# Performance work log

Hardware: AMD Instinct MI355X
Metric: run time of the kernel (lower is better)

Reference implementation:

```python
import jax, jax.numpy as jnp
import numpy as np

NUM_RULES = 256
IN_F = 2048
OUT_F = 2048
RANK = 8
BLOCK = 64
NUM_BLOCKS = min(IN_F, OUT_F) // BLOCK  # 32
SHARED_RANK = int(round(np.sqrt(min(IN_F, OUT_F))))  # 45
N = 16384


def setup_inputs() -> dict:
    key = jax.random.key(0)
    ks = jax.random.split(key, 7)
    x = jax.random.normal(ks[0], (N, IN_F), dtype=jnp.float32)
    rule_ids = jax.random.randint(ks[1], (N,), 0, NUM_RULES, dtype=jnp.int32)
    shared_in = jax.random.normal(ks[2], (IN_F, SHARED_RANK), dtype=jnp.float32) * (1.0 / np.sqrt(IN_F))
    shared_out = jax.random.normal(ks[3], (SHARED_RANK, OUT_F), dtype=jnp.float32) * (1.0 / np.sqrt(SHARED_RANK))
    rule_in = jax.random.normal(ks[4], (NUM_RULES, BLOCK, RANK), dtype=jnp.float32) * (1.0 / np.sqrt(BLOCK))
    rule_out = jax.random.normal(ks[5], (NUM_RULES, RANK, BLOCK), dtype=jnp.float32) * (1.0 / np.sqrt(RANK))
    rule_block_logits = jax.random.normal(ks[6], (NUM_RULES, NUM_BLOCKS), dtype=jnp.float32) * (1.0 / np.sqrt(NUM_BLOCKS))
    return {"x": x, "rule_ids": rule_ids, "shared_in": shared_in, "shared_out": shared_out,
            "rule_in": rule_in, "rule_out": rule_out, "rule_block_logits": rule_block_logits}


def reference(x, rule_ids, shared_in, shared_out, rule_in, rule_out, rule_block_logits):
    # Shared low-rank path: [N, in] @ [in, r] @ [r, out]
    base_out = (x @ shared_in) @ shared_out  # [N, OUT_F]

    total = NUM_BLOCKS * BLOCK
    x_blocks = x[:, :total].reshape(-1, NUM_BLOCKS, BLOCK)  # [N, B, bs]

    # Per-token gather of rule adapter params. This is mathematically
    # identical to the torch sort/pad/bmm/scatter path (zero padding
    # contributes zero), expressed as a dense gather + batched einsum.
    r_in = rule_in[rule_ids]    # [N, bs, RANK]
    r_out = rule_out[rule_ids]  # [N, RANK, bs]
    hidden = jnp.einsum('nbs,nsr->nbr', x_blocks, r_in)     # [N, B, RANK]
    adapter = jnp.einsum('nbr,nrs->nbs', hidden, r_out)     # [N, B, bs]

    # Block selector softmax with temperature 1/sqrt(num_blocks)
    inv_temp = jnp.sqrt(jnp.float32(NUM_BLOCKS))
    sel = jax.nn.softmax(rule_block_logits[rule_ids] * inv_temp, axis=-1)  # [N, B]
    weighted = (adapter * sel[:, :, None]).reshape(-1, total)  # [N, total]

    adapter_full = jnp.zeros_like(base_out).at[:, :total].set(weighted.astype(base_out.dtype))
    return base_out + adapter_full
```

## Files before the change

kernel.cpp:

```cpp
#include <hip/hip_runtime.h>
#include <hip/hip_bf16.h>
#include <math.h>

#define NTOK  16384
#define INF   2048
#define OUTF  2048
#define SR    45
#define RANK  8
#define BLK   64
#define NBLK  32
#define NRULE 256
#define NHIST 32
#define MAXSLOT (NTOK + NRULE * 15)
#define NTILE32 (MAXSLOT / 32)

typedef __attribute__((ext_vector_type(8))) short bf16x8;
typedef __attribute__((ext_vector_type(4))) float f32x4;
typedef __attribute__((ext_vector_type(4))) short s16x4;

typedef const __attribute__((address_space(1))) unsigned int GU32;
typedef __attribute__((address_space(3))) unsigned int LU32;

#define MFMA __builtin_amdgcn_mfma_f32_16x16x32_bf16
#define SBAR() __builtin_amdgcn_sched_barrier(0)

__device__ inline short f2bs(float f) {
    __hip_bfloat16 h = __float2bfloat16(f);
    return *reinterpret_cast<short*>(&h);
}
__device__ inline bf16x8 cvt8(const float4& a, const float4& b) {
    bf16x8 r;
    r[0] = f2bs(a.x); r[1] = f2bs(a.y); r[2] = f2bs(a.z); r[3] = f2bs(a.w);
    r[4] = f2bs(b.x); r[5] = f2bs(b.y); r[6] = f2bs(b.z); r[7] = f2bs(b.w);
    return r;
}

__global__ void kprep_a(const int* __restrict__ rule_ids,
                        const float* __restrict__ shared_in,
                        const float* __restrict__ shared_out,
                        const float* __restrict__ rule_in,
                        const float* __restrict__ rule_out,
                        unsigned short* __restrict__ ssb,
                        unsigned short* __restrict__ sob,
                        unsigned short* __restrict__ rinf,
                        unsigned short* __restrict__ rof,
                        int* __restrict__ ghist_part,
                        int* __restrict__ perm_p,
                        int* __restrict__ srid_p)
{
    if (blockIdx.x < 128) {
        const int tid = blockIdx.x * 256 + threadIdx.x;
        const int stride = 128 * 256;
        for (int idx = tid; idx < 64 * 3 * 512; idx += stride) {
            int ch = idx / 1536, rem = idx - ch * 1536;
            int nf = rem / 512;
            int l = (rem >> 3) & 63, j = idx & 7;
            int k = ch * 32 + ((l >> 4) << 3) + j;
            int col = nf * 16 + (l & 15);
            ssb[idx] = (col < SR) ? (unsigned short)f2bs(shared_in[(size_t)k * SR + col]) : 0;
        }
        for (int idx = tid; idx < 128 * 2 * 512; idx += stride) {
            int CF = idx >> 10;
            int kc = (idx >> 9) & 1;
            int l = (idx >> 3) & 63, j = idx & 7;
            int k = kc * 32 + ((l >> 4) << 3) + j;
            int col = CF * 16 + (l & 15);
            sob[idx] = (k < SR) ? (unsigned short)f2bs(shared_out[(size_t)k * OUTF + col]) : 0;
        }
        for (int idx = tid; idx < NRULE * 2 * 512; idx += stride) {
            int rid = idx >> 10;
            int half = (idx >> 9) & 1;
            int l = (idx >> 3) & 63, j = idx & 7;
            int r = l & 15;
            int s = half * 32 + ((l >> 4) << 3) + j;
            rinf[idx] = (r < RANK) ? (unsigned short)f2bs(rule_in[(size_t)rid * 512 + s * RANK + r]) : 0;
        }
        for (int idx = tid; idx < NRULE * 4 * 512; idx += stride) {
            int rid = idx >> 11;
            int cf = (idx >> 9) & 3;
            int l = (idx >> 3) & 63, j = idx & 7;
            int k = ((l >> 4) << 3) + j;
            int c = cf * 16 + (l & 15);
            rof[idx] = (k < RANK) ? (unsigned short)f2bs(rule_out[(size_t)rid * 512 + k * BLK + c]) : 0;
        }
    } else {
        __shared__ int lh[NRULE];
        const int tid = threadIdx.x;
        const int hb = blockIdx.x - 128;
        lh[tid] = 0;
        __syncthreads();
        const int base = hb * 512;
        atomicAdd(&lh[rule_ids[base + tid]], 1);
        atomicAdd(&lh[rule_ids[base + 256 + tid]], 1);
        __syncthreads();
        ghist_part[hb * NRULE + tid] = lh[tid];
        for (int j = tid; j < MAXSLOT / 32; j += 256) {
            int idx = hb * (MAXSLOT / 32) + j;
            perm_p[idx] = -1;
            srid_p[idx] = 0;
        }
    }
}

__global__ void kprep_scan(const int* __restrict__ ghist_part,
                           const float* __restrict__ logits,
                           int* __restrict__ gcnt,
                           int* __restrict__ srid_p,
                           float* __restrict__ sel_t,
                           int* __restrict__ ntot)
{
    __shared__ int sc[NRULE];
    const int tid = threadIdx.x;
    int h = 0;
#pragma unroll
    for (int b = 0; b < NHIST; ++b) h += ghist_part[b * NRULE + tid];
    const int pd = (h + 15) & ~15;
    sc[tid] = pd;
    for (int off = 1; off < NRULE; off <<= 1) {
        __syncthreads();
        int v = (tid >= off) ? sc[tid - off] : 0;
        __syncthreads();
        sc[tid] += v;
    }
    __syncthreads();
    const int excl = sc[tid] - pd;
    gcnt[tid] = excl;
    for (int q = h; q < pd; ++q) srid_p[excl + q] = tid;
    if (tid == NRULE - 1) *ntot = sc[tid];
    const float invT = 5.65685424949238f;
    const float* __restrict__ lg = logits + (size_t)tid * NBLK;
    float m = -1e30f;
    for (int b = 0; b < NBLK; ++b) m = fmaxf(m, lg[b] * invT);
    float s = 0.0f;
    for (int b = 0; b < NBLK; ++b) s += expf(lg[b] * invT - m);
    const float inv = 1.0f / s;
    for (int b = 0; b < NBLK; ++b)
        sel_t[(size_t)tid * NBLK + b] = expf(lg[b] * invT - m) * inv;
}

__global__ void kprep_scatter(const int* __restrict__ rule_ids,
                              int* __restrict__ gcnt,
                              int* __restrict__ perm_p,
                              int* __restrict__ srid_p)
{
    const int i = blockIdx.x * 256 + threadIdx.x;
    const int r = rule_ids[i];
    const int p = atomicAdd(&gcnt[r], 1);
    perm_p[p] = i;
    srid_p[p] = r;
}

__global__ __launch_bounds__(256, 4)
void kmain(const float* __restrict__ x,
           const int* __restrict__ perm_p,
           const int* __restrict__ srid_p,
           const unsigned short* __restrict__ ssb,
           const unsigned short* __restrict__ sob,
           const unsigned short* __restrict__ rinf,
           const unsigned short* __restrict__ rof,
           const float* __restrict__ sel_t,
           const int* __restrict__ ntot,
           float* __restrict__ out)
{
    __shared__ __align__(16) float xbuf[2][2048];
    __shared__ __align__(16) unsigned short hs_lds[2][16][264];
    __shared__ __align__(16) char pool[4608];

#define HST(PB, S, KH, SL, R) \
    (((float*)pool)[(((((PB) * 2 + (S)) * 2 + (KH)) * 16 + (SL)) * 8) + (R)])
#define TBF(SL, C) (((unsigned short*)pool)[(SL) * 72 + (C)])
#define TRD(W, SL, C) (((float*)xbuf)[(((W) * 16 + (SL)) * 52) + (C)])

    const int slot0 = blockIdx.x * 32;
    if (slot0 >= *ntot) return;

    const int tid  = threadIdx.x;
    const int lane = tid & 63;
    const int w    = tid >> 6;
    const int s    = w & 1;
    const int kh   = w >> 1;
    const int row_l = lane & 15, grp = lane >> 4;
    const int slotbase = slot0 + s * 16;

    const int rid_u = __builtin_amdgcn_readfirstlane(srid_p[slotbase]);

    const int r0 = tid >> 4;
    const int u  = tid & 15;
    int tokA = perm_p[slot0 + r0];       if (tokA < 0) tokA = 0;
    int tokB = perm_p[slot0 + r0 + 16];  if (tokB < 0) tokB = 0;
    const char* gA = (const char*)(x + (size_t)tokA * INF) + ((u ^ (r0 & 7)) << 4);
    const char* gB = (const char*)(x + (size_t)tokB * INF) + ((u ^ (r0 & 7)) << 4);

#define STAGE(CH) do { \
        char* _lb = (char*)xbuf + (((CH) & 1) << 13) + (w << 10); \
        const size_t _o = (size_t)(CH) << 8; \
        __builtin_amdgcn_global_load_lds((GU32*)(gA + _o), (LU32*)_lb,          16, 0, 0); \
        __builtin_amdgcn_global_load_lds((GU32*)(gB + _o), (LU32*)(_lb + 4096), 16, 0, 0); \
    } while (0)

    const int rphys = s * 16 + row_l;
    const int offA = (rphys * 16 + ((kh * 8 + grp * 2 + 0) ^ (row_l & 7))) << 4;
    const int offB = (rphys * 16 + ((kh * 8 + grp * 2 + 1) ^ (row_l & 7))) << 4;

    const bf16x8 ri = *(const bf16x8*)(rinf + ((size_t)rid_u * 2 + kh) * 512 + lane * 8);

    f32x4 aT0 = {0.f, 0.f, 0.f, 0.f};
    f32x4 aT1 = {0.f, 0.f, 0.f, 0.f};
    f32x4 aT2 = {0.f, 0.f, 0.f, 0.f};

    STAGE(0);
    __syncthreads();

    for (int ch = 0; ch < 32; ++ch) {
        if (ch < 31) STAGE(ch + 1);

        if (ch > 0) {
            const int b = ch - 1, pb = b & 1;
            const int sl = kh * 8 + (lane >> 3), r = lane & 7;
            const float v = HST(pb, s, 0, sl, r) + HST(pb, s, 1, sl, r);
            hs_lds[s][sl][b * 8 + r] =
                (unsigned short)f2bs(v * sel_t[(size_t)rid_u * NBLK + b]);
        }

        {
            const char* xb = (const char*)xbuf + ((ch & 1) << 13);
            const float4 fa = *(const float4*)(xb + offA);
            const float4 fb = *(const float4*)(xb + offB);
            const bf16x8 af = cvt8(fa, fb);
            const unsigned short* sp = ssb + (size_t)(ch * 2 + kh) * 1536 + lane * 8;
            f32x4 aH = {0.f, 0.f, 0.f, 0.f};
            aT0 = MFMA(af, *(const bf16x8*)(sp),        aT0, 0, 0, 0);
            aT1 = MFMA(af, *(const bf16x8*)(sp + 512),  aT1, 0, 0, 0);
            aT2 = MFMA(af, *(const bf16x8*)(sp + 1024), aT2, 0, 0, 0);
            aH  = MFMA(af, ri, aH, 0, 0, 0);
            if (row_l < RANK) {
#pragma unroll
                for (int q = 0; q < 4; ++q)
                    HST(ch & 1, s, kh, (grp << 2) + q, row_l) = aH[q];
            }
        }
        __syncthreads();
    }

    {
        const int b = 31, pb = 1;
        const int sl = kh * 8 + (lane >> 3), r = lane & 7;
        const float v = HST(pb, s, 0, sl, r) + HST(pb, s, 1, sl, r);
        hs_lds[s][sl][b * 8 + r] =
            (unsigned short)f2bs(v * sel_t[(size_t)rid_u * NBLK + b]);
    }
#pragma unroll
    for (int q = 0; q < 4; ++q) {
        const int sl = (grp << 2) + q;
        TRD(w, sl, row_l)      = aT0[q];
        TRD(w, sl, 16 + row_l) = aT1[q];
        TRD(w, sl, 32 + row_l) = aT2[q];
    }
    __syncthreads();
    {
        const int sl = tid >> 3;
        const int st = sl >> 4, tk = sl & 15;
        const int cidx = tid & 7;
        if (cidx < 6) {
            const int c0 = cidx << 3;
            s16x4 v0, v1;
#pragma unroll
            for (int j = 0; j < 4; ++j) {
                v0[j] = f2bs(TRD(st, tk, c0 + j)     + TRD(st + 2, tk, c0 + j));
                v1[j] = f2bs(TRD(st, tk, c0 + 4 + j) + TRD(st + 2, tk, c0 + 4 + j));
            }
            *(s16x4*)(&TBF(sl, c0))     = v0;
            *(s16x4*)(&TBF(sl, c0 + 4)) = v1;
        } else {
            const int c0 = 48 + ((cidx - 6) << 3);
            const s16x4 z = {0, 0, 0, 0};
            *(s16x4*)(&TBF(sl, c0))     = z;
            *(s16x4*)(&TBF(sl, c0 + 4)) = z;
        }
    }
    __syncthreads();

    {
        const int p = kh;
        const bf16x8 at0 = *(const bf16x8*)(&TBF(s * 16 + row_l, grp << 3));
        const bf16x8 at1 = *(const bf16x8*)(&TBF(s * 16 + row_l, 32 + (grp << 3)));

        bf16x8 rfv[4];
#pragma unroll
        for (int i = 0; i < 4; ++i)
            rfv[i] = *(const bf16x8*)(rof + ((size_t)rid_u * 4 + i) * 512 + lane * 8);

        const int4 pv = *(const int4*)(perm_p + slotbase + (grp << 2));
        float* const orow0 = out + (size_t)pv.x * OUTF;
        float* const orow1 = out + (size_t)pv.y * OUTF;
        float* const orow2 = out + (size_t)pv.z * OUTF;
        float* const orow3 = out + (size_t)pv.w * OUTF;

        const int CF0 = p * 64;
        const int bb0 = p * 16;
        const unsigned short* __restrict__ sobw = sob + (size_t)CF0 * 1024 + lane * 8;

        bf16x8 sb[4][2];
        bf16x8 ah[2];
        const bf16x8 zz = {0, 0, 0, 0, 0, 0, 0, 0};

#define LOADQ(SL, QI) do { \
        const unsigned short* _sp = sobw + (size_t)(QI) * 1024; \
        sb[SL][0] = *(const bf16x8*)(_sp); \
        sb[SL][1] = *(const bf16x8*)(_sp + 512); \
    } while (0)
#define LOADA(SL, BI) do { \
        ah[SL] = zz; \
        if (lane < 16) \
            ah[SL] = *(const bf16x8*)(&hs_lds[s][lane][(bb0 + (BI)) * 8]); \
    } while (0)

        LOADQ(0, 0); LOADQ(1, 1); LOADQ(2, 2);
        LOADA(0, 0);
        SBAR();

#pragma unroll
        for (int qi = 0; qi < 64; ++qi) {
            if (qi < 61) LOADQ((qi + 3) & 3, qi + 3);
            if ((qi & 3) == 0 && qi < 60) LOADA(((qi >> 2) + 1) & 1, (qi >> 2) + 1);
            SBAR();
            f32x4 acc = {0.f, 0.f, 0.f, 0.f};
            acc = MFMA(at0, sb[qi & 3][0], acc, 0, 0, 0);
            acc = MFMA(at1, sb[qi & 3][1], acc, 0, 0, 0);
            acc = MFMA(ah[(qi >> 2) & 1], rfv[qi & 3], acc, 0, 0, 0);
            const int col = ((CF0 + qi) << 4) + row_l;
            if (pv.x >= 0) orow0[col] = acc[0];
            if (pv.y >= 0) orow1[col] = acc[1];
            if (pv.z >= 0) orow2[col] = acc[2];
            if (pv.w >= 0) orow3[col] = acc[3];
            SBAR();
        }
#undef LOADQ
#undef LOADA
    }
}

extern "C" void kernel_launch(void* const* d_in, const int* in_sizes, int n_in,
                              void* d_out, int out_size, void* d_ws, size_t ws_size,
                              hipStream_t stream)
{
    const float* x          = (const float*)d_in[0];
    const int*   rule_ids   = (const int*)  d_in[1];
    const float* shared_in  = (const float*)d_in[2];
    const float* shared_out = (const float*)d_in[3];
    const float* rule_in    = (const float*)d_in[4];
    const float* rule_out   = (const float*)d_in[5];
    const float* logits     = (const float*)d_in[6];
    float* out = (float*)d_out;

    char* p = (char*)d_ws;
    auto carve = [&p](size_t bytes) {
        char* r = p;
        p += (bytes + 255) & ~(size_t)255;
        return r;
    };
    int*            perm_p = (int*)carve(MAXSLOT * 4);
    int*            srid_p = (int*)carve(MAXSLOT * 4);
    unsigned short* ssb    = (unsigned short*)carve(64 * 3 * 512 * 2);
    unsigned short* sob    = (unsigned short*)carve(128 * 2 * 512 * 2);
    unsigned short* rinf   = (unsigned short*)carve((size_t)NRULE * 2 * 512 * 2);
    unsigned short* rof    = (unsigned short*)carve((size_t)NRULE * 4 * 512 * 2);
    float*          sel_t  = (float*)carve((size_t)NRULE * NBLK * 4);
    int*            ghistp = (int*)carve((size_t)NHIST * NRULE * 4);
    int*            gcnt   = (int*)carve(NRULE * 4);
    int*            ntot   = (int*)carve(4);

    kprep_a<<<dim3(160), dim3(256), 0, stream>>>(
        rule_ids, shared_in, shared_out, rule_in, rule_out,
        ssb, sob, rinf, rof, ghistp, perm_p, srid_p);
    kprep_scan<<<dim3(1), dim3(256), 0, stream>>>(
        ghistp, logits, gcnt, srid_p, sel_t, ntot);
    kprep_scatter<<<dim3(64), dim3(256), 0, stream>>>(
        rule_ids, gcnt, perm_p, srid_p);
    kmain<<<dim3(NTILE32), dim3(256), 0, stream>>>(
        x, perm_p, srid_p, ssb, sob, rinf, rof, sel_t, ntot, out);
}
```

Measured before the change: 94.30 us.

## Triple-buffer x staging, split chunks by wave parity, manual vmcnt pipelining

The first phase now uses a 3-deep LDS ring for x chunks. Each wave pair takes alternate chunks and computes both K-halves itself, so the cross-wave hidden-state reduction through LDS goes away. Shared-in weights are prefetched into registers two chunks ahead with inline-asm loads and explicit s_waitcnt vmcnt counts. The output phase replaces the per-row store predicates with redirection to a dummy row. This is meant to cut barriers and hide load latency, but it lowers the occupancy target from 4 to 3 blocks and depends on fragile hand-counted vmcnt values.

```diff
diff --git a/kernel.cpp b/kernel.cpp
--- a/kernel.cpp
+++ b/kernel.cpp
@@ -23,6 +23,14 @@
 
 #define MFMA __builtin_amdgcn_mfma_f32_16x16x32_bf16
 #define SBAR() __builtin_amdgcn_sched_barrier(0)
+
+#define VMCNT(n) do { asm volatile("s_waitcnt vmcnt(" #n ")" ::: "memory"); \
+                      __builtin_amdgcn_sched_barrier(0); } while (0)
+#define BAR()    do { __builtin_amdgcn_sched_barrier(0); \
+                      __builtin_amdgcn_s_barrier(); \
+                      __builtin_amdgcn_sched_barrier(0); } while (0)
+#define GLOAD(dst, ptr) \
+    asm volatile("global_load_dwordx4 %0, %1, off" : "=v"(dst) : "v"(ptr) : "memory")
 
 __device__ inline short f2bs(float f) {
     __hip_bfloat16 h = __float2bfloat16(f);
@@ -150,7 +158,7 @@
     srid_p[p] = r;
 }
 
-__global__ __launch_bounds__(256, 4)
+__global__ __launch_bounds__(256, 3)
 void kmain(const float* __restrict__ x,
            const int* __restrict__ perm_p,
            const int* __restrict__ srid_p,
@@ -160,15 +168,13 @@
            const unsigned short* __restrict__ rof,
            const float* __restrict__ sel_t,
            const int* __restrict__ ntot,
+           float* __restrict__ dummy,
            float* __restrict__ out)
 {
-    __shared__ __align__(16) float xbuf[2][2048];
+    __shared__ __align__(16) float xbuf[3][2048];
     __shared__ __align__(16) unsigned short hs_lds[2][16][264];
-    __shared__ __align__(16) char pool[4608];
-
-#define HST(PB, S, KH, SL, R) \
-    (((float*)pool)[(((((PB) * 2 + (S)) * 2 + (KH)) * 16 + (SL)) * 8) + (R)])
-#define TBF(SL, C) (((unsigned short*)pool)[(SL) * 72 + (C)])
+    __shared__ __align__(16) unsigned short t_bf[32][72];
+
 #define TRD(W, SL, C) (((float*)xbuf)[(((W) * 16 + (SL)) * 52) + (C)])
 
     const int slot0 = blockIdx.x * 32;
@@ -178,7 +184,7 @@
     const int lane = tid & 63;
     const int w    = tid >> 6;
     const int s    = w & 1;
-    const int kh   = w >> 1;
+    const int par  = w >> 1;
     const int row_l = lane & 15, grp = lane >> 4;
     const int slotbase = slot0 + s * 16;
 
@@ -189,66 +195,82 @@
     int tokA = perm_p[slot0 + r0];       if (tokA < 0) tokA = 0;
     int tokB = perm_p[slot0 + r0 + 16];  if (tokB < 0) tokB = 0;
     const char* gA = (const char*)(x + (size_t)tokA * INF) + ((u ^ (r0 & 7)) << 4);
-    const char* gB = (const char*)(x + (size_t)tokB * INF) + ((u ^ (r0 & 7)) << 4);
+    const char* gB = (const char*)(x + (size_t)tokB * INF) + (((u ^ ((r0 + 16) & 7))) << 4);
 
 #define STAGE(CH) do { \
-        char* _lb = (char*)xbuf + (((CH) & 1) << 13) + (w << 10); \
+        char* _lb = (char*)xbuf + (size_t)((CH) % 3) * 8192 + (w << 10); \
         const size_t _o = (size_t)(CH) << 8; \
         __builtin_amdgcn_global_load_lds((GU32*)(gA + _o), (LU32*)_lb,          16, 0, 0); \
         __builtin_amdgcn_global_load_lds((GU32*)(gB + _o), (LU32*)(_lb + 4096), 16, 0, 0); \
     } while (0)
 
     const int rphys = s * 16 + row_l;
-    const int offA = (rphys * 16 + ((kh * 8 + grp * 2 + 0) ^ (row_l & 7))) << 4;
-    const int offB = (rphys * 16 + ((kh * 8 + grp * 2 + 1) ^ (row_l & 7))) << 4;
-
-    const bf16x8 ri = *(const bf16x8*)(rinf + ((size_t)rid_u * 2 + kh) * 512 + lane * 8);
+#define XOFF(Q, E) ((rphys * 16 + ((((Q) * 8) + grp * 2 + (E)) ^ (row_l & 7))) << 4)
+    const int off00 = XOFF(0, 0), off01 = XOFF(0, 1);
+    const int off10 = XOFF(1, 0), off11 = XOFF(1, 1);
+
+    const unsigned short* __restrict__ sbase = ssb + lane * 8;
+
+    bf16x8 ri0, ri1;
+    GLOAD(ri0, rinf + ((size_t)rid_u * 2 + 0) * 512 + lane * 8);
+    GLOAD(ri1, rinf + ((size_t)rid_u * 2 + 1) * 512 + lane * 8);
 
     f32x4 aT0 = {0.f, 0.f, 0.f, 0.f};
     f32x4 aT1 = {0.f, 0.f, 0.f, 0.f};
     f32x4 aT2 = {0.f, 0.f, 0.f, 0.f};
 
-    STAGE(0);
-    __syncthreads();
-
+    bf16x8 wreg[2][6];
+
+#define WLOAD(SLOT, CH) do { \
+        const unsigned short* _wp = sbase + (size_t)(CH) * 3072; \
+        GLOAD(wreg[SLOT][0], _wp); \
+        GLOAD(wreg[SLOT][1], _wp + 512); \
+        GLOAD(wreg[SLOT][2], _wp + 1024); \
+        GLOAD(wreg[SLOT][3], _wp + 1536); \
+        GLOAD(wreg[SLOT][4], _wp + 2048); \
+        GLOAD(wreg[SLOT][5], _wp + 2560); \
+    } while (0)
+
+    STAGE(0); STAGE(1);
+    if (par == 0) WLOAD(0, 0); else WLOAD(0, 1);
+
+#pragma unroll
     for (int ch = 0; ch < 32; ++ch) {
-        if (ch < 31) STAGE(ch + 1);
-
-        if (ch > 0) {
-            const int b = ch - 1, pb = b & 1;
-            const int sl = kh * 8 + (lane >> 3), r = lane & 7;
-            const float v = HST(pb, s, 0, sl, r) + HST(pb, s, 1, sl, r);
-            hs_lds[s][sl][b * 8 + r] =
-                (unsigned short)f2bs(v * sel_t[(size_t)rid_u * NBLK + b]);
-        }
-
-        {
-            const char* xb = (const char*)xbuf + ((ch & 1) << 13);
-            const float4 fa = *(const float4*)(xb + offA);
-            const float4 fb = *(const float4*)(xb + offB);
-            const bf16x8 af = cvt8(fa, fb);
-            const unsigned short* sp = ssb + (size_t)(ch * 2 + kh) * 1536 + lane * 8;
+        if (ch < 30) STAGE(ch + 2);
+        const bool mine = ((ch & 1) == par);
+        if (mine) { if (ch < 30) VMCNT(4);  else if (ch == 30) VMCNT(2); else VMCNT(0); }
+        else      { if (ch < 30) VMCNT(10); else if (ch == 30) VMCNT(8); else VMCNT(0); }
+        BAR();
+        if (mine) {
+            const int slot = (ch >> 1) & 1;
+            const char* xb = (const char*)xbuf + (size_t)(ch % 3) * 8192;
+            const float4 fa0 = *(const float4*)(xb + off00);
+            const float4 fa1 = *(const float4*)(xb + off01);
+            const float4 fb0 = *(const float4*)(xb + off10);
+            const float4 fb1 = *(const float4*)(xb + off11);
+            const bf16x8 af0 = cvt8(fa0, fa1);
+            const bf16x8 af1 = cvt8(fb0, fb1);
             f32x4 aH = {0.f, 0.f, 0.f, 0.f};
-            aT0 = MFMA(af, *(const bf16x8*)(sp),        aT0, 0, 0, 0);
-            aT1 = MFMA(af, *(const bf16x8*)(sp + 512),  aT1, 0, 0, 0);
-            aT2 = MFMA(af, *(const bf16x8*)(sp + 1024), aT2, 0, 0, 0);
-            aH  = MFMA(af, ri, aH, 0, 0, 0);
+            aT0 = MFMA(af0, wreg[slot][0], aT0, 0, 0, 0);
+            aT1 = MFMA(af0, wreg[slot][1], aT1, 0, 0, 0);
+            aT2 = MFMA(af0, wreg[slot][2], aT2, 0, 0, 0);
+            aH  = MFMA(af0, ri0, aH, 0, 0, 0);
+            aT0 = MFMA(af1, wreg[slot][3], aT0, 0, 0, 0);
+            aT1 = MFMA(af1, wreg[slot][4], aT1, 0, 0, 0);
+            aT2 = MFMA(af1, wreg[slot][5], aT2, 0, 0, 0);
+            aH  = MFMA(af1, ri1, aH, 0, 0, 0);
+            if (ch + 2 < 32) WLOAD(slot ^ 1, ch + 2);
+            const float sel = sel_t[(size_t)rid_u * NBLK + ch];
             if (row_l < RANK) {
 #pragma unroll
                 for (int q = 0; q < 4; ++q)
-                    HST(ch & 1, s, kh, (grp << 2) + q, row_l) = aH[q];
+                    hs_lds[s][(grp << 2) + q][ch * 8 + row_l] =
+                        (unsigned short)f2bs(aH[q] * sel);
             }
         }
-        __syncthreads();
-    }
-
-    {
-        const int b = 31, pb = 1;
-        const int sl = kh * 8 + (lane >> 3), r = lane & 7;
-        const float v = HST(pb, s, 0, sl, r) + HST(pb, s, 1, sl, r);
-        hs_lds[s][sl][b * 8 + r] =
-            (unsigned short)f2bs(v * sel_t[(size_t)rid_u * NBLK + b]);
-    }
+        BAR();
+    }
+
 #pragma unroll
     for (int q = 0; q < 4; ++q) {
         const int sl = (grp << 2) + q;
@@ -269,32 +291,32 @@
                 v0[j] = f2bs(TRD(st, tk, c0 + j)     + TRD(st + 2, tk, c0 + j));
                 v1[j] = f2bs(TRD(st, tk, c0 + 4 + j) + TRD(st + 2, tk, c0 + 4 + j));
             }
-            *(s16x4*)(&TBF(sl, c0))     = v0;
-            *(s16x4*)(&TBF(sl, c0 + 4)) = v1;
+            *(s16x4*)(&t_bf[sl][c0])     = v0;
+            *(s16x4*)(&t_bf[sl][c0 + 4]) = v1;
         } else {
             const int c0 = 48 + ((cidx - 6) << 3);
             const s16x4 z = {0, 0, 0, 0};
-            *(s16x4*)(&TBF(sl, c0))     = z;
-            *(s16x4*)(&TBF(sl, c0 + 4)) = z;
+            *(s16x4*)(&t_bf[sl][c0])     = z;
+            *(s16x4*)(&t_bf[sl][c0 + 4]) = z;
         }
     }
     __syncthreads();
 
     {
-        const int p = kh;
-        const bf16x8 at0 = *(const bf16x8*)(&TBF(s * 16 + row_l, grp << 3));
-        const bf16x8 at1 = *(const bf16x8*)(&TBF(s * 16 + row_l, 32 + (grp << 3)));
+        const int p = par;
+        const bf16x8 at0 = *(const bf16x8*)(&t_bf[s * 16 + row_l][grp << 3]);
+        const bf16x8 at1 = *(const bf16x8*)(&t_bf[s * 16 + row_l][32 + (grp << 3)]);
 
         bf16x8 rfv[4];
 #pragma unroll
         for (int i = 0; i < 4; ++i)
-            rfv[i] = *(const bf16x8*)(rof + ((size_t)rid_u * 4 + i) * 512 + lane * 8);
+            GLOAD(rfv[i], rof + ((size_t)rid_u * 4 + i) * 512 + lane * 8);
 
         const int4 pv = *(const int4*)(perm_p + slotbase + (grp << 2));
-        float* const orow0 = out + (size_t)pv.x * OUTF;
-        float* const orow1 = out + (size_t)pv.y * OUTF;
-        float* const orow2 = out + (size_t)pv.z * OUTF;
-        float* const orow3 = out + (size_t)pv.w * OUTF;
+        float* const orow0 = (pv.x < 0) ? dummy : out + (size_t)pv.x * OUTF;
+        float* const orow1 = (pv.y < 0) ? dummy : out + (size_t)pv.y * OUTF;
+        float* const orow2 = (pv.z < 0) ? dummy : out + (size_t)pv.z * OUTF;
+        float* const orow3 = (pv.w < 0) ? dummy : out + (size_t)pv.w * OUTF;
 
         const int CF0 = p * 64;
         const int bb0 = p * 16;
@@ -304,10 +326,9 @@
         bf16x8 ah[2];
         const bf16x8 zz = {0, 0, 0, 0, 0, 0, 0, 0};
 
-#define LOADQ(SL, QI) do { \
-        const unsigned short* _sp = sobw + (size_t)(QI) * 1024; \
-        sb[SL][0] = *(const bf16x8*)(_sp); \
-        sb[SL][1] = *(const bf16x8*)(_sp + 512); \
+#define SLOADQ(SL, QI) do { \
+        GLOAD(sb[SL][0], sobw + (size_t)(QI) * 1024); \
+        GLOAD(sb[SL][1], sobw + (size_t)(QI) * 1024 + 512); \
     } while (0)
 #define LOADA(SL, BI) do { \
         ah[SL] = zz; \
@@ -315,27 +336,31 @@
             ah[SL] = *(const bf16x8*)(&hs_lds[s][lane][(bb0 + (BI)) * 8]); \
     } while (0)
 
-        LOADQ(0, 0); LOADQ(1, 1); LOADQ(2, 2);
+        SLOADQ(0, 0); SLOADQ(1, 1); SLOADQ(2, 2);
         LOADA(0, 0);
-        SBAR();
 
 #pragma unroll
         for (int qi = 0; qi < 64; ++qi) {
-            if (qi < 61) LOADQ((qi + 3) & 3, qi + 3);
+            if (qi < 61) SLOADQ((qi + 3) & 3, qi + 3);
             if ((qi & 3) == 0 && qi < 60) LOADA(((qi >> 2) + 1) & 1, (qi >> 2) + 1);
-            SBAR();
+            if (qi == 0)       VMCNT(6);
+            else if (qi == 1)  VMCNT(10);
+            else if (qi == 2)  VMCNT(14);
+            else if (qi <= 60) VMCNT(18);
+            else if (qi == 61) VMCNT(16);
+            else if (qi == 62) VMCNT(14);
+            else               VMCNT(12);
             f32x4 acc = {0.f, 0.f, 0.f, 0.f};
             acc = MFMA(at0, sb[qi & 3][0], acc, 0, 0, 0);
             acc = MFMA(at1, sb[qi & 3][1], acc, 0, 0, 0);
             acc = MFMA(ah[(qi >> 2) & 1], rfv[qi & 3], acc, 0, 0, 0);
             const int col = ((CF0 + qi) << 4) + row_l;
-            if (pv.x >= 0) orow0[col] = acc[0];
-            if (pv.y >= 0) orow1[col] = acc[1];
-            if (pv.z >= 0) orow2[col] = acc[2];
-            if (pv.w >= 0) orow3[col] = acc[3];
-            SBAR();
-        }
-#undef LOADQ
+            orow0[col] = acc[0];
+            orow1[col] = acc[1];
+            orow2[col] = acc[2];
+            orow3[col] = acc[3];
+        }
+#undef SLOADQ
 #undef LOADA
     }
 }
@@ -369,6 +394,7 @@
     int*            ghistp = (int*)carve((size_t)NHIST * NRULE * 4);
     int*            gcnt   = (int*)carve(NRULE * 4);
     int*            ntot   = (int*)carve(4);
+    float*          dummy  = (float*)carve((size_t)OUTF * 4);
 
     kprep_a<<<dim3(160), dim3(256), 0, stream>>>(
         rule_ids, shared_in, shared_out, rule_in, rule_out,
@@ -378,5 +404,5 @@
     kprep_scatter<<<dim3(64), dim3(256), 0, stream>>>(
         rule_ids, gcnt, perm_p, srid_p);
     kmain<<<dim3(NTILE32), dim3(256), 0, stream>>>(
-        x, perm_p, srid_p, ssb, sob, rinf, rof, sel_t, ntot, out);
-}
+        x, perm_p, srid_p, ssb, sob, rinf, rof, sel_t, ntot, dummy, out);
+}
```

Result: no change. 95.72 us (+1.5%).
